# Performance work log

Measured on AMD Instinct MI355X. Metric: run time of the kernel, lower is better.

The kernel has to match this reference:

```python
import jax, jax.numpy as jnp
import numpy as np

N_NODES = 1_000_000
N_EDGES = 32_000_000
DC = 16
HIDDEN = 32
EPS = 1e-8
LN_EPS = 1e-5


def _harmonic_encoding(x, dC):
    # x: [n] curvature in [-1,1]; returns [n, dC] (dC even here)
    norm = jnp.clip((x + 1.0) / (2.0 + EPS), 0.0, 1.0)
    freqs = jnp.arange(1, dC // 2 + 1, dtype=x.dtype) * jnp.pi  # [dC/2]
    ang = norm[:, None] * freqs[None, :]                        # [n, dC/2]
    # interleave sin/cos exactly like torch.stack(...,dim=2).view(n,dC)
    return jnp.stack([jnp.sin(ang), jnp.cos(ang)], axis=2).reshape(x.shape[0], dC)


def setup_inputs() -> dict:
    key = jax.random.key(0)
    k_orc, k_ei, k_w1, k_w2, k_g = jax.random.split(key, 5)
    node_orc = jax.random.uniform(k_orc, (N_NODES,), dtype=jnp.float32) * 2.0 - 1.0
    edge_index = jax.random.randint(k_ei, (2, N_EDGES), 0, N_NODES, dtype=jnp.int64)
    # MLP params (torch Linear convention: W [out, in])
    W1 = jax.random.normal(k_w1, (HIDDEN, DC), dtype=jnp.float32) * (1.0 / np.sqrt(DC))
    b1 = jnp.zeros((HIDDEN,), dtype=jnp.float32)
    W2 = jax.random.normal(k_w2, (DC, HIDDEN), dtype=jnp.float32) * (1.0 / np.sqrt(HIDDEN))
    b2 = jnp.zeros((DC,), dtype=jnp.float32)
    gamma = jnp.ones((DC,), dtype=jnp.float32)
    beta = jnp.zeros((DC,), dtype=jnp.float32)
    return {"node_orc": node_orc, "edge_index": edge_index,
            "W1": W1, "b1": b1, "W2": W2, "b2": b2,
            "gamma": gamma, "beta": beta}


def _neighbor_mean(node_orc, edge_index):
    src, dst = edge_index[0], edge_index[1]
    n = node_orc.shape[0]
    deg = jnp.zeros((n,), node_orc.dtype).at[src].add(1.0).at[dst].add(1.0)
    s = (jnp.zeros((n,), node_orc.dtype)
         .at[src].add(node_orc[dst])
         .at[dst].add(node_orc[src]))
    return jnp.where(deg > 0, s / jnp.where(deg > 0, deg, 1.0), 0.0)


def reference(node_orc, edge_index, W1, b1, W2, b2, gamma, beta):
    # advanced harmonic encoding: node encoding + neighbor-mean encoding
    nb_mean = _neighbor_mean(node_orc, edge_index)
    Phi_base = jnp.concatenate(
        [_harmonic_encoding(node_orc, DC // 2),
         _harmonic_encoding(nb_mean, DC // 2)], axis=1)      # [n, 16]
    # learnable MLP (dropout in eval = identity) + LayerNorm + residual
    h = jax.nn.relu(jnp.einsum('nd,hd->nh', Phi_base, W1) + b1)
    y = jnp.einsum('nh,dh->nd', h, W2) + b2
    mu = jnp.mean(y, axis=-1, keepdims=True)
    var = jnp.var(y, axis=-1, keepdims=True)
    y = (y - mu) / jnp.sqrt(var + LN_EPS) * gamma + beta
    return y + Phi_base
```

## Files before the change

kernel.cpp:

```cpp
#include <hip/hip_runtime.h>

constexpr int kNodes = 1000000;
constexpr int kEdges = 32000000;

constexpr int NB = 256;
constexpr int BSHIFT = 12;
constexpr int BNODES = 4096;
constexpr int NBUSED = (kNodes + BNODES - 1) / BNODES;
constexpr int EPT = 4096;
constexpr int LSIZE = 8960;
constexpr int TILES = (kEdges + EPT - 1) / EPT;
constexpr int CAP = 284672;
constexpr int SPLIT = 2;
constexpr unsigned PADREC = 0x10000000u;

constexpr size_t kArenaBytes = (size_t)NBUSED * CAP * 4;
constexpr size_t kCurOff    = kArenaBytes;
constexpr size_t kCurBytes  = (size_t)NB * 64;
constexpr size_t kAccOff    = kCurOff + kCurBytes;
constexpr size_t kAccBytes  = (size_t)SPLIT * kNodes * 4;
constexpr size_t kOrcqOff   = kAccOff + kAccBytes;
constexpr size_t kOrcqBytes = (size_t)kNodes * 2;
constexpr size_t kWsNeeded  = kOrcqOff + kOrcqBytes;

__global__ __launch_bounds__(256) void quant_orc(
        const float* __restrict__ orc, unsigned short* __restrict__ orcq,
        unsigned* __restrict__ gcur) {
    if (blockIdx.x == 0 && threadIdx.x < NB) gcur[threadIdx.x * 16] = 0u;
    const int i = (blockIdx.x * 256 + threadIdx.x) * 4;
    if (i >= kNodes) return;
    const float4 v = *reinterpret_cast<const float4*>(orc + i);
    unsigned q0 = __float2uint_rn((v.x + 1.0f) * 32768.0f);
    unsigned q1 = __float2uint_rn((v.y + 1.0f) * 32768.0f);
    unsigned q2 = __float2uint_rn((v.z + 1.0f) * 32768.0f);
    unsigned q3 = __float2uint_rn((v.w + 1.0f) * 32768.0f);
    q0 = q0 > 65535u ? 65535u : q0;
    q1 = q1 > 65535u ? 65535u : q1;
    q2 = q2 > 65535u ? 65535u : q2;
    q3 = q3 > 65535u ? 65535u : q3;
    ushort4 q;
    q.x = (unsigned short)q0; q.y = (unsigned short)q1;
    q.z = (unsigned short)q2; q.w = (unsigned short)q3;
    *reinterpret_cast<ushort4*>(orcq + i) = q;
}

__global__ __launch_bounds__(1024) void scatter_sort(
        const int* __restrict__ ei, const unsigned short* __restrict__ orcq,
        unsigned* __restrict__ arena, unsigned* __restrict__ gcur) {
    __shared__ alignas(16) unsigned reorder[LSIZE];
    __shared__ unsigned char gb[LSIZE / 4];
    __shared__ unsigned cnt[NB];
    __shared__ unsigned pend[NB];
    __shared__ unsigned dstadd[NB];
    const int tid = threadIdx.x;
    const int t = blockIdx.x;
    const int e0 = t * EPT;
    const int ne = min(EPT, kEdges - e0);
    const int k4 = tid * 4;

    if (tid < NB) cnt[tid] = 0u;
    __syncthreads();

    int4 s4, d4;
    s4.x = s4.y = s4.z = s4.w = 0; d4 = s4;
    unsigned pq0 = 0, pq1 = 0, pq2 = 0, pq3 = 0;
    const bool act = k4 < ne;
    if (act) {
        s4 = *reinterpret_cast<const int4*>(ei + e0 + k4);
        d4 = *reinterpret_cast<const int4*>(ei + kEdges + e0 + k4);
        const unsigned a0 = orcq[d4.x], a1 = orcq[d4.y],
                       a2 = orcq[d4.z], a3 = orcq[d4.w];
        const unsigned b0 = orcq[s4.x], b1 = orcq[s4.y],
                       b2 = orcq[s4.z], b3 = orcq[s4.w];
        atomicAdd(&cnt[(unsigned)s4.x >> BSHIFT], 1u);
        atomicAdd(&cnt[(unsigned)s4.y >> BSHIFT], 1u);
        atomicAdd(&cnt[(unsigned)s4.z >> BSHIFT], 1u);
        atomicAdd(&cnt[(unsigned)s4.w >> BSHIFT], 1u);
        atomicAdd(&cnt[(unsigned)d4.x >> BSHIFT], 1u);
        atomicAdd(&cnt[(unsigned)d4.y >> BSHIFT], 1u);
        atomicAdd(&cnt[(unsigned)d4.z >> BSHIFT], 1u);
        atomicAdd(&cnt[(unsigned)d4.w >> BSHIFT], 1u);
        pq0 = a0 | (b0 << 16);
        pq1 = a1 | (b1 << 16);
        pq2 = a2 | (b2 << 16);
        pq3 = a3 | (b3 << 16);
    }
    __syncthreads();

    unsigned P0 = 0, P1 = 0, P2 = 0, P3 = 0;
    unsigned g0 = 0, g1 = 0, g2 = 0, g3 = 0;
    unsigned pc0 = 0, pc1 = 0, pc2 = 0, pc3 = 0;
    if (tid < 64) {
        const unsigned c0 = cnt[4 * tid + 0], c1 = cnt[4 * tid + 1];
        const unsigned c2 = cnt[4 * tid + 2], c3 = cnt[4 * tid + 3];
        pc0 = (c0 + 3u) & ~3u; pc1 = (c1 + 3u) & ~3u;
        pc2 = (c2 + 3u) & ~3u; pc3 = (c3 + 3u) & ~3u;
        const unsigned loc = pc0 + pc1 + pc2 + pc3;
        unsigned inc = loc;
        #pragma unroll
        for (int o = 1; o < 64; o <<= 1) {
            const unsigned v = (unsigned)__shfl_up((int)inc, o, 64);
            if (tid >= o) inc += v;
        }
        P0 = inc - loc; P1 = P0 + pc0; P2 = P1 + pc1; P3 = P2 + pc2;
        cnt[4 * tid + 0] = P0; pend[4 * tid + 0] = P1;
        cnt[4 * tid + 1] = P1; pend[4 * tid + 1] = P2;
        cnt[4 * tid + 2] = P2; pend[4 * tid + 2] = P3;
        cnt[4 * tid + 3] = P3; pend[4 * tid + 3] = P3 + pc3;
        g0 = atomicAdd(&gcur[(4 * tid + 0) * 16], pc0);
        g1 = atomicAdd(&gcur[(4 * tid + 1) * 16], pc1);
        g2 = atomicAdd(&gcur[(4 * tid + 2) * 16], pc2);
        g3 = atomicAdd(&gcur[(4 * tid + 3) * 16], pc3);
    }
    __syncthreads();

    if (act) {
        #define RANK1(S, D, PQ) { \
            const unsigned bs_ = (unsigned)(S) >> BSHIFT; \
            const unsigned rs_ = atomicAdd(&cnt[bs_], 1u); \
            reorder[rs_] = (((unsigned)(S) & (BNODES - 1)) << 16) | ((PQ) & 0xFFFFu); \
            gb[rs_ >> 2] = (unsigned char)bs_; \
            const unsigned bd_ = (unsigned)(D) >> BSHIFT; \
            const unsigned rd_ = atomicAdd(&cnt[bd_], 1u); \
            reorder[rd_] = (((unsigned)(D) & (BNODES - 1)) << 16) | ((PQ) >> 16); \
            gb[rd_ >> 2] = (unsigned char)bd_; }
        RANK1(s4.x, d4.x, pq0)
        RANK1(s4.y, d4.y, pq1)
        RANK1(s4.z, d4.z, pq2)
        RANK1(s4.w, d4.w, pq3)
        #undef RANK1
    }
    __syncthreads();

    if (tid < 64) {
        if (g0 + pc0 > (unsigned)CAP) g0 = CAP - pc0;
        if (g1 + pc1 > (unsigned)CAP) g1 = CAP - pc1;
        if (g2 + pc2 > (unsigned)CAP) g2 = CAP - pc2;
        if (g3 + pc3 > (unsigned)CAP) g3 = CAP - pc3;
        dstadd[4 * tid + 0] = (unsigned)(4 * tid + 0) * CAP + g0 - P0;
        dstadd[4 * tid + 1] = (unsigned)(4 * tid + 1) * CAP + g1 - P1;
        dstadd[4 * tid + 2] = (unsigned)(4 * tid + 2) * CAP + g2 - P2;
        dstadd[4 * tid + 3] = (unsigned)(4 * tid + 3) * CAP + g3 - P3;
    }
    if (tid < NB) {
        const unsigned e = pend[tid];
        for (unsigned k = cnt[tid]; k < e; ++k) reorder[k] = PADREC;
    }
    __syncthreads();

    const unsigned tot = pend[NB - 1];
    for (unsigned k = (unsigned)k4; k < tot; k += 4096) {
        const unsigned bb = gb[k >> 2];
        *reinterpret_cast<int4*>(arena + dstadd[bb] + k) =
            *reinterpret_cast<const int4*>(reorder + k);
    }
}

__global__ __launch_bounds__(1024) void bucket_accum(
        const unsigned* __restrict__ arena, const unsigned* __restrict__ gcur,
        unsigned* __restrict__ acc) {
    __shared__ unsigned lacc[BNODES + 4];
    const int tid = threadIdx.x;
    const int b = blockIdx.x >> 1;
    const int half = blockIdx.x & 1;
    for (int k = tid; k < BNODES + 4; k += 1024) lacc[k] = 0u;
    __syncthreads();
    const unsigned len = gcur[b * 16];
    const unsigned h = (len >> 1) & ~3u;
    const unsigned lo4 = (half ? h : 0u) >> 2;
    const unsigned hi4 = (half ? len : h) >> 2;
    const uint4* __restrict__ p =
        reinterpret_cast<const uint4*>(arena + (size_t)b * CAP);
    for (unsigned i = lo4 + tid; i < hi4; i += 1024) {
        const uint4 v = p[i];
        atomicAdd(&lacc[v.x >> 16], (v.x & 0xFFFFu) | 0x1000000u);
        atomicAdd(&lacc[v.y >> 16], (v.y & 0xFFFFu) | 0x1000000u);
        atomicAdd(&lacc[v.z >> 16], (v.z & 0xFFFFu) | 0x1000000u);
        atomicAdd(&lacc[v.w >> 16], (v.w & 0xFFFFu) | 0x1000000u);
    }
    __syncthreads();
    const int base = b << BSHIFT;
    unsigned* __restrict__ dst = acc + (size_t)half * kNodes;
    for (int k = tid; k < BNODES; k += 1024) {
        const int nn = base + k;
        if (nn < kNodes) dst[nn] = lacc[k];
    }
}

constexpr float kScale = 1048576.0f;
constexpr float kInvScale = 1.0f / 1048576.0f;
constexpr long long kBias = 1ll << 36;

__global__ __launch_bounds__(256) void zero_acc(unsigned long long* __restrict__ acc) {
    int i = blockIdx.x * 256 + threadIdx.x;
    if (i < kNodes) acc[i] = 0ull;
}

__global__ __launch_bounds__(256) void edge_kernel(
        const int* __restrict__ ei,
        const float* __restrict__ orc,
        unsigned long long* __restrict__ acc) {
    int t = blockIdx.x * 256 + threadIdx.x;
    int e0 = t * 4;
    if (e0 >= kEdges) return;
    const int4 s4 = *reinterpret_cast<const int4*>(ei + e0);
    const int4 d4 = *reinterpret_cast<const int4*>(ei + kEdges + e0);
    const int ss[4] = {s4.x, s4.y, s4.z, s4.w};
    const int dd[4] = {d4.x, d4.y, d4.z, d4.w};
    #pragma unroll
    for (int k = 0; k < 4; ++k) {
        const float os = orc[ss[k]];
        const float od = orc[dd[k]];
        const unsigned long long ps =
            (1ull << 48) + (unsigned long long)(kBias + (long long)__float2ll_rn(od * kScale));
        const unsigned long long pd =
            (1ull << 48) + (unsigned long long)(kBias + (long long)__float2ll_rn(os * kScale));
        atomicAdd(&acc[ss[k]], ps);
        atomicAdd(&acc[dd[k]], pd);
    }
}

template <int MODE>
__global__ __launch_bounds__(256) void node_kernel(
        const float* __restrict__ orc,
        const unsigned long long* __restrict__ acc64,
        const unsigned* __restrict__ acc32,
        const float* __restrict__ W1, const float* __restrict__ b1,
        const float* __restrict__ W2, const float* __restrict__ b2,
        const float* __restrict__ gamma, const float* __restrict__ beta,
        float* __restrict__ out) {
    const int i = blockIdx.x * 256 + threadIdx.x;
    if (i >= kNodes) return;

    const float x0 = orc[i];
    float nb;
    if (MODE == 0) {
        const unsigned long long p = acc64[i];
        const unsigned deg = (unsigned)(p >> 48);
        const long long sf = (long long)(p & ((1ull << 48) - 1)) - (long long)deg * kBias;
        const float s = (float)sf * kInvScale;
        nb = (deg > 0) ? s / (float)deg : 0.0f;
    } else {
        const unsigned p0 = acc32[i];
        const unsigned p1 = acc32[kNodes + i];
        const unsigned deg = (p0 >> 24) + (p1 >> 24);
        const unsigned sumq = (p0 & 0xFFFFFFu) + (p1 & 0xFFFFFFu);
        nb = (deg > 0)
            ? ((float)sumq * (1.0f / 32768.0f) / (float)deg - 1.0f) : 0.0f;
    }

    constexpr float kPi = 3.14159265358979323846f;
    float Phi[16];
    const float n0 = __saturatef((x0 + 1.0f) * 0.5f);
    const float n1 = __saturatef((nb + 1.0f) * 0.5f);
    #pragma unroll
    for (int k = 0; k < 4; ++k) {
        const float a0 = n0 * (float)(k + 1) * kPi;
        const float a1 = n1 * (float)(k + 1) * kPi;
        Phi[2 * k]     = __sinf(a0);
        Phi[2 * k + 1] = __cosf(a0);
        Phi[8 + 2 * k]     = __sinf(a1);
        Phi[8 + 2 * k + 1] = __cosf(a1);
    }

    float y[16];
    #pragma unroll
    for (int d = 0; d < 16; ++d) y[d] = b2[d];
    #pragma unroll
    for (int j = 0; j < 32; ++j) {
        float a = b1[j];
        #pragma unroll
        for (int d = 0; d < 16; ++d) a = fmaf(Phi[d], W1[j * 16 + d], a);
        a = fmaxf(a, 0.0f);
        #pragma unroll
        for (int d = 0; d < 16; ++d) y[d] = fmaf(a, W2[d * 32 + j], y[d]);
    }

    float mu = 0.0f;
    #pragma unroll
    for (int d = 0; d < 16; ++d) mu += y[d];
    mu *= (1.0f / 16.0f);
    float var = 0.0f;
    #pragma unroll
    for (int d = 0; d < 16; ++d) { const float t = y[d] - mu; var = fmaf(t, t, var); }
    var *= (1.0f / 16.0f);
    const float inv = rsqrtf(var + 1e-5f);

    float4* o4 = reinterpret_cast<float4*>(out + (size_t)i * 16);
    #pragma unroll
    for (int q = 0; q < 4; ++q) {
        float4 o;
        o.x = (y[4 * q + 0] - mu) * inv * gamma[4 * q + 0] + beta[4 * q + 0] + Phi[4 * q + 0];
        o.y = (y[4 * q + 1] - mu) * inv * gamma[4 * q + 1] + beta[4 * q + 1] + Phi[4 * q + 1];
        o.z = (y[4 * q + 2] - mu) * inv * gamma[4 * q + 2] + beta[4 * q + 2] + Phi[4 * q + 2];
        o.w = (y[4 * q + 3] - mu) * inv * gamma[4 * q + 3] + beta[4 * q + 3] + Phi[4 * q + 3];
        o4[q] = o;
    }
}

extern "C" void kernel_launch(void* const* d_in, const int* in_sizes, int n_in,
                              void* d_out, int out_size, void* d_ws, size_t ws_size,
                              hipStream_t stream) {
    const float* orc   = (const float*)d_in[0];
    const int*   ei    = (const int*)d_in[1];
    const float* W1    = (const float*)d_in[2];
    const float* b1    = (const float*)d_in[3];
    const float* W2    = (const float*)d_in[4];
    const float* b2    = (const float*)d_in[5];
    const float* gamma = (const float*)d_in[6];
    const float* beta  = (const float*)d_in[7];
    float* out = (float*)d_out;
    char* ws = (char*)d_ws;

    if (ws_size >= kWsNeeded) {
        unsigned* arena = (unsigned*)ws;
        unsigned* gcur = (unsigned*)(ws + kCurOff);
        unsigned* acc = (unsigned*)(ws + kAccOff);
        unsigned short* orcq = (unsigned short*)(ws + kOrcqOff);
        quant_orc<<<(kNodes / 4 + 255) / 256, 256, 0, stream>>>(orc, orcq, gcur);
        scatter_sort<<<TILES, 1024, 0, stream>>>(ei, orcq, arena, gcur);
        bucket_accum<<<NBUSED * SPLIT, 1024, 0, stream>>>(arena, gcur, acc);
        node_kernel<3><<<(kNodes + 255) / 256, 256, 0, stream>>>(
            orc, nullptr, acc, W1, b1, W2, b2, gamma, beta, out);
    } else {
        unsigned long long* acc = (unsigned long long*)ws;
        zero_acc<<<(kNodes + 255) / 256, 256, 0, stream>>>(acc);
        edge_kernel<<<(kEdges / 4 + 255) / 256, 256, 0, stream>>>(ei, orc, acc);
        node_kernel<0><<<(kNodes + 255) / 256, 256, 0, stream>>>(
            orc, acc, nullptr, W1, b1, W2, b2, gamma, beta, out);
    }
}
```

Baseline: 728.0 us.

## Replace prefix-sum tile reorder with fixed per-bucket slabs and overflow list

```diff
diff --git a/kernel.cpp b/kernel.cpp
--- a/kernel.cpp
+++ b/kernel.cpp
@@ -8,25 +8,32 @@
 constexpr int BNODES = 4096;
 constexpr int NBUSED = (kNodes + BNODES - 1) / BNODES;
 constexpr int EPT = 4096;
-constexpr int LSIZE = 8960;
 constexpr int TILES = (kEdges + EPT - 1) / EPT;
+constexpr int SLOT = 72;
+constexpr int GP = SLOT / 4;
 constexpr int CAP = 284672;
 constexpr int SPLIT = 2;
 constexpr unsigned PADREC = 0x10000000u;
+constexpr unsigned OVFCAP = 8192;
 
 constexpr size_t kArenaBytes = (size_t)NBUSED * CAP * 4;
 constexpr size_t kCurOff    = kArenaBytes;
-constexpr size_t kCurBytes  = (size_t)NB * 64;
+constexpr size_t kCurBytes  = (size_t)NB * 64 + 64;
 constexpr size_t kAccOff    = kCurOff + kCurBytes;
 constexpr size_t kAccBytes  = (size_t)SPLIT * kNodes * 4;
 constexpr size_t kOrcqOff   = kAccOff + kAccBytes;
 constexpr size_t kOrcqBytes = (size_t)kNodes * 2;
-constexpr size_t kWsNeeded  = kOrcqOff + kOrcqBytes;
+constexpr size_t kOvfOff    = (kOrcqOff + kOrcqBytes + 7) & ~(size_t)7;
+constexpr size_t kOvfBytes  = (size_t)OVFCAP * 8;
+constexpr size_t kWsNeeded  = kOvfOff + kOvfBytes;
 
 __global__ __launch_bounds__(256) void quant_orc(
         const float* __restrict__ orc, unsigned short* __restrict__ orcq,
         unsigned* __restrict__ gcur) {
-    if (blockIdx.x == 0 && threadIdx.x < NB) gcur[threadIdx.x * 16] = 0u;
+    if (blockIdx.x == 0) {
+        if (threadIdx.x < NB) gcur[threadIdx.x * 16] = 0u;
+        if (threadIdx.x == 0) gcur[NB * 16] = 0u;
+    }
     const int i = (blockIdx.x * 256 + threadIdx.x) * 4;
     if (i >= kNodes) return;
     const float4 v = *reinterpret_cast<const float4*>(orc + i);
@@ -46,11 +53,11 @@
 
 __global__ __launch_bounds__(1024) void scatter_sort(
         const int* __restrict__ ei, const unsigned short* __restrict__ orcq,
-        unsigned* __restrict__ arena, unsigned* __restrict__ gcur) {
-    __shared__ alignas(16) unsigned reorder[LSIZE];
-    __shared__ unsigned char gb[LSIZE / 4];
+        unsigned* __restrict__ arena, unsigned* __restrict__ gcur,
+        unsigned long long* __restrict__ ovf) {
+    __shared__ alignas(16) unsigned slab[NB * SLOT];
     __shared__ unsigned cnt[NB];
-    __shared__ unsigned pend[NB];
+    __shared__ unsigned pcs[NB];
     __shared__ unsigned dstadd[NB];
     const int tid = threadIdx.x;
     const int t = blockIdx.x;
@@ -61,111 +68,64 @@
     if (tid < NB) cnt[tid] = 0u;
     __syncthreads();
 
-    int4 s4, d4;
-    s4.x = s4.y = s4.z = s4.w = 0; d4 = s4;
-    unsigned pq0 = 0, pq1 = 0, pq2 = 0, pq3 = 0;
-    const bool act = k4 < ne;
-    if (act) {
-        s4 = *reinterpret_cast<const int4*>(ei + e0 + k4);
-        d4 = *reinterpret_cast<const int4*>(ei + kEdges + e0 + k4);
+    if (k4 < ne) {
+        const int4 s4 = *reinterpret_cast<const int4*>(ei + e0 + k4);
+        const int4 d4 = *reinterpret_cast<const int4*>(ei + kEdges + e0 + k4);
         const unsigned a0 = orcq[d4.x], a1 = orcq[d4.y],
                        a2 = orcq[d4.z], a3 = orcq[d4.w];
         const unsigned b0 = orcq[s4.x], b1 = orcq[s4.y],
                        b2 = orcq[s4.z], b3 = orcq[s4.w];
-        atomicAdd(&cnt[(unsigned)s4.x >> BSHIFT], 1u);
-        atomicAdd(&cnt[(unsigned)s4.y >> BSHIFT], 1u);
-        atomicAdd(&cnt[(unsigned)s4.z >> BSHIFT], 1u);
-        atomicAdd(&cnt[(unsigned)s4.w >> BSHIFT], 1u);
-        atomicAdd(&cnt[(unsigned)d4.x >> BSHIFT], 1u);
-        atomicAdd(&cnt[(unsigned)d4.y >> BSHIFT], 1u);
-        atomicAdd(&cnt[(unsigned)d4.z >> BSHIFT], 1u);
-        atomicAdd(&cnt[(unsigned)d4.w >> BSHIFT], 1u);
-        pq0 = a0 | (b0 << 16);
-        pq1 = a1 | (b1 << 16);
-        pq2 = a2 | (b2 << 16);
-        pq3 = a3 | (b3 << 16);
-    }
-    __syncthreads();
-
-    unsigned P0 = 0, P1 = 0, P2 = 0, P3 = 0;
-    unsigned g0 = 0, g1 = 0, g2 = 0, g3 = 0;
-    unsigned pc0 = 0, pc1 = 0, pc2 = 0, pc3 = 0;
-    if (tid < 64) {
-        const unsigned c0 = cnt[4 * tid + 0], c1 = cnt[4 * tid + 1];
-        const unsigned c2 = cnt[4 * tid + 2], c3 = cnt[4 * tid + 3];
-        pc0 = (c0 + 3u) & ~3u; pc1 = (c1 + 3u) & ~3u;
-        pc2 = (c2 + 3u) & ~3u; pc3 = (c3 + 3u) & ~3u;
-        const unsigned loc = pc0 + pc1 + pc2 + pc3;
-        unsigned inc = loc;
-        #pragma unroll
-        for (int o = 1; o < 64; o <<= 1) {
-            const unsigned v = (unsigned)__shfl_up((int)inc, o, 64);
-            if (tid >= o) inc += v;
+        #define RANK1(N, Q) { \
+            const unsigned b_ = (unsigned)(N) >> BSHIFT; \
+            const unsigned r_ = atomicAdd(&cnt[b_], 1u); \
+            if (r_ < (unsigned)SLOT) { \
+                slab[b_ * SLOT + r_] = (((unsigned)(N) & (BNODES - 1)) << 16) | (Q); \
+            } else { \
+                const unsigned oi_ = atomicAdd(&gcur[NB * 16], 1u); \
+                if (oi_ < OVFCAP) \
+                    ovf[oi_] = ((unsigned long long)(unsigned)(N) << 16) | (Q); \
+            } }
+        RANK1(s4.x, a0) RANK1(s4.y, a1) RANK1(s4.z, a2) RANK1(s4.w, a3)
+        RANK1(d4.x, b0) RANK1(d4.y, b1) RANK1(d4.z, b2) RANK1(d4.w, b3)
+        #undef RANK1
+    }
+    __syncthreads();
+
+    if (tid < NB) {
+        unsigned c = cnt[tid];
+        c = c > (unsigned)SLOT ? (unsigned)SLOT : c;
+        const unsigned pc = (c + 3u) & ~3u;
+        pcs[tid] = pc;
+        unsigned g = atomicAdd(&gcur[tid * 16], pc);
+        if (g + pc > (unsigned)CAP) g = CAP - pc;
+        dstadd[tid] = (unsigned)tid * CAP + g;
+        for (unsigned j = c; j < pc; ++j) slab[tid * SLOT + j] = PADREC;
+    }
+    __syncthreads();
+
+    for (int k = tid; k < NB * GP; k += 1024) {
+        const int b = k / GP;
+        const int g4 = (k - b * GP) * 4;
+        if ((unsigned)g4 < pcs[b]) {
+            *reinterpret_cast<int4*>(arena + dstadd[b] + g4) =
+                *reinterpret_cast<const int4*>(slab + b * SLOT + g4);
         }
-        P0 = inc - loc; P1 = P0 + pc0; P2 = P1 + pc1; P3 = P2 + pc2;
-        cnt[4 * tid + 0] = P0; pend[4 * tid + 0] = P1;
-        cnt[4 * tid + 1] = P1; pend[4 * tid + 1] = P2;
-        cnt[4 * tid + 2] = P2; pend[4 * tid + 2] = P3;
-        cnt[4 * tid + 3] = P3; pend[4 * tid + 3] = P3 + pc3;
-        g0 = atomicAdd(&gcur[(4 * tid + 0) * 16], pc0);
-        g1 = atomicAdd(&gcur[(4 * tid + 1) * 16], pc1);
-        g2 = atomicAdd(&gcur[(4 * tid + 2) * 16], pc2);
-        g3 = atomicAdd(&gcur[(4 * tid + 3) * 16], pc3);
-    }
-    __syncthreads();
-
-    if (act) {
-        #define RANK1(S, D, PQ) { \
-            const unsigned bs_ = (unsigned)(S) >> BSHIFT; \
-            const unsigned rs_ = atomicAdd(&cnt[bs_], 1u); \
-            reorder[rs_] = (((unsigned)(S) & (BNODES - 1)) << 16) | ((PQ) & 0xFFFFu); \
-            gb[rs_ >> 2] = (unsigned char)bs_; \
-            const unsigned bd_ = (unsigned)(D) >> BSHIFT; \
-            const unsigned rd_ = atomicAdd(&cnt[bd_], 1u); \
-            reorder[rd_] = (((unsigned)(D) & (BNODES - 1)) << 16) | ((PQ) >> 16); \
-            gb[rd_ >> 2] = (unsigned char)bd_; }
-        RANK1(s4.x, d4.x, pq0)
-        RANK1(s4.y, d4.y, pq1)
-        RANK1(s4.z, d4.z, pq2)
-        RANK1(s4.w, d4.w, pq3)
-        #undef RANK1
-    }
-    __syncthreads();
-
-    if (tid < 64) {
-        if (g0 + pc0 > (unsigned)CAP) g0 = CAP - pc0;
-        if (g1 + pc1 > (unsigned)CAP) g1 = CAP - pc1;
-        if (g2 + pc2 > (unsigned)CAP) g2 = CAP - pc2;
-        if (g3 + pc3 > (unsigned)CAP) g3 = CAP - pc3;
-        dstadd[4 * tid + 0] = (unsigned)(4 * tid + 0) * CAP + g0 - P0;
-        dstadd[4 * tid + 1] = (unsigned)(4 * tid + 1) * CAP + g1 - P1;
-        dstadd[4 * tid + 2] = (unsigned)(4 * tid + 2) * CAP + g2 - P2;
-        dstadd[4 * tid + 3] = (unsigned)(4 * tid + 3) * CAP + g3 - P3;
-    }
-    if (tid < NB) {
-        const unsigned e = pend[tid];
-        for (unsigned k = cnt[tid]; k < e; ++k) reorder[k] = PADREC;
-    }
-    __syncthreads();
-
-    const unsigned tot = pend[NB - 1];
-    for (unsigned k = (unsigned)k4; k < tot; k += 4096) {
-        const unsigned bb = gb[k >> 2];
-        *reinterpret_cast<int4*>(arena + dstadd[bb] + k) =
-            *reinterpret_cast<const int4*>(reorder + k);
     }
 }
 
 __global__ __launch_bounds__(1024) void bucket_accum(
         const unsigned* __restrict__ arena, const unsigned* __restrict__ gcur,
         unsigned* __restrict__ acc) {
-    __shared__ unsigned lacc[BNODES + 4];
+    __shared__ unsigned lacc[2][BNODES + 4];
     const int tid = threadIdx.x;
     const int b = blockIdx.x >> 1;
     const int half = blockIdx.x & 1;
-    for (int k = tid; k < BNODES + 4; k += 1024) lacc[k] = 0u;
-    __syncthreads();
-    const unsigned len = gcur[b * 16];
+    for (int k = tid; k < 2 * (BNODES + 4); k += 1024)
+        lacc[0][k] = 0u;
+    __syncthreads();
+    unsigned* __restrict__ my = lacc[(tid >> 6) & 1];
+    unsigned len = gcur[b * 16];
+    len = len > (unsigned)CAP ? (unsigned)CAP : len;
     const unsigned h = (len >> 1) & ~3u;
     const unsigned lo4 = (half ? h : 0u) >> 2;
     const unsigned hi4 = (half ? len : h) >> 2;
@@ -173,17 +133,29 @@
         reinterpret_cast<const uint4*>(arena + (size_t)b * CAP);
     for (unsigned i = lo4 + tid; i < hi4; i += 1024) {
         const uint4 v = p[i];
-        atomicAdd(&lacc[v.x >> 16], (v.x & 0xFFFFu) | 0x1000000u);
-        atomicAdd(&lacc[v.y >> 16], (v.y & 0xFFFFu) | 0x1000000u);
-        atomicAdd(&lacc[v.z >> 16], (v.z & 0xFFFFu) | 0x1000000u);
-        atomicAdd(&lacc[v.w >> 16], (v.w & 0xFFFFu) | 0x1000000u);
+        atomicAdd(&my[v.x >> 16], (v.x & 0xFFFFu) | 0x1000000u);
+        atomicAdd(&my[v.y >> 16], (v.y & 0xFFFFu) | 0x1000000u);
+        atomicAdd(&my[v.z >> 16], (v.z & 0xFFFFu) | 0x1000000u);
+        atomicAdd(&my[v.w >> 16], (v.w & 0xFFFFu) | 0x1000000u);
     }
     __syncthreads();
     const int base = b << BSHIFT;
     unsigned* __restrict__ dst = acc + (size_t)half * kNodes;
     for (int k = tid; k < BNODES; k += 1024) {
         const int nn = base + k;
-        if (nn < kNodes) dst[nn] = lacc[k];
+        if (nn < kNodes) dst[nn] = lacc[0][k] + lacc[1][k];
+    }
+}
+
+__global__ __launch_bounds__(256) void ovf_fix(
+        const unsigned long long* __restrict__ ovf,
+        const unsigned* __restrict__ gcur, unsigned* __restrict__ acc) {
+    unsigned n = gcur[NB * 16];
+    n = n > OVFCAP ? OVFCAP : n;
+    for (unsigned i = threadIdx.x; i < n; i += 256) {
+        const unsigned long long v = ovf[i];
+        atomicAdd(&acc[(unsigned)(v >> 16)],
+                  ((unsigned)v & 0xFFFFu) | 0x1000000u);
     }
 }
 
@@ -317,9 +289,11 @@
         unsigned* gcur = (unsigned*)(ws + kCurOff);
         unsigned* acc = (unsigned*)(ws + kAccOff);
         unsigned short* orcq = (unsigned short*)(ws + kOrcqOff);
+        unsigned long long* ovf = (unsigned long long*)(ws + kOvfOff);
         quant_orc<<<(kNodes / 4 + 255) / 256, 256, 0, stream>>>(orc, orcq, gcur);
-        scatter_sort<<<TILES, 1024, 0, stream>>>(ei, orcq, arena, gcur);
+        scatter_sort<<<TILES, 1024, 0, stream>>>(ei, orcq, arena, gcur, ovf);
         bucket_accum<<<NBUSED * SPLIT, 1024, 0, stream>>>(arena, gcur, acc);
+        ovf_fix<<<1, 256, 0, stream>>>(ovf, gcur, acc);
         node_kernel<3><<<(kNodes + 255) / 256, 256, 0, stream>>>(
             orc, nullptr, acc, W1, b1, W2, b2, gamma, beta, out);
     } else {
```

Measured after the change: 708.9 us. -2.6%, faster.
